# Kernel optimization log

Measured on AMD Instinct MI355X. Metric: run time of the kernel, lower is better.

## Reference

```python
import jax, jax.numpy as jnp
import numpy as np

K = 16  # top-k affinities kept per current-frame pixel (init arg k)


def setup_inputs() -> dict:
    key = jax.random.key(0)
    k1, k2 = jax.random.split(key)
    B, C, H, W = 2, 256, 64, 64
    N = H * W
    cur_prev_aff = jax.random.normal(k1, (B, N, N), dtype=jnp.float32)
    feat = jax.random.normal(k2, (B, C, H, W), dtype=jnp.float32)
    return {"cur_prev_aff": cur_prev_aff, "feat": feat}


def reference(cur_prev_aff, feat):
    # cur_prev_aff: [B, N, N] affinity from each current pixel i to each prev pixel j
    # feat:         [B, C, H, W] previous-frame features, N = H*W
    B, C, H, W = feat.shape
    N = H * W
    # top-k affinity masking per current pixel
    vals, idx = jax.lax.top_k(cur_prev_aff, K)      # [B, N, K]
    w = jax.nn.softmax(vals, axis=-1)               # normalized masked affinities (masked_cpa)
    # gather prev-frame features at top-k locations and weighted-sum
    feat_t = feat.reshape(B, C, N).transpose(0, 2, 1)        # [B, N, C]
    gathered = jax.vmap(lambda f, ix: f[ix])(feat_t, idx)    # [B, N, K, C]
    out = jnp.einsum('bnk,bnkc->bnc', w, gathered)           # [B, N, C]
    return out.transpose(0, 2, 1).reshape(B, C, H, W)
```

## Files before the change

kernel.cpp:

```cpp
#include <hip/hip_runtime.h>

#define N_PIX 4096
#define N_CH 256
#define KSEL 16

__device__ __forceinline__ unsigned f2key(float f) {
  unsigned u = __float_as_uint(f);
  return u ^ ((unsigned)((int)u >> 31) | 0x80000000u);
}
__device__ __forceinline__ float key2f(unsigned k) {
  unsigned u = (k & 0x80000000u) ? (k ^ 0x80000000u) : ~k;
  return __uint_as_float(u);
}
__device__ __forceinline__ unsigned umax2(unsigned a, unsigned b) { return a > b ? a : b; }

__global__ void transpose_feat_kernel(const float* __restrict__ feat,
                                      float* __restrict__ feat_t) {
  __shared__ float tile[32][33];
  const int b = blockIdx.z;
  const int n0 = blockIdx.x * 32;
  const int c0 = blockIdx.y * 32;
  const int tx = threadIdx.x, ty = threadIdx.y;
  const float* src = feat + (size_t)b * N_CH * N_PIX;
  float* dst = feat_t + (size_t)b * N_PIX * N_CH;
#pragma unroll
  for (int j = 0; j < 32; j += 8)
    tile[ty + j][tx] = src[(size_t)(c0 + ty + j) * N_PIX + n0 + tx];
  __syncthreads();
#pragma unroll
  for (int j = 0; j < 32; j += 8)
    dst[(size_t)(n0 + ty + j) * N_CH + c0 + tx] = tile[tx][ty + j];
}

template <bool FT>
__global__ __launch_bounds__(256, 3) void topk_wave_kernel(
    const float* __restrict__ aff, const float* __restrict__ feat,
    float* __restrict__ out) {
  __shared__ unsigned s_ck[4][64];
  __shared__ unsigned s_cj[4][64];
  __shared__ uint2 s_wj[4][KSEL];
  __shared__ float s_out[4][N_CH];

  const int tid = threadIdx.x;
  const int lane = tid & 63;
  const int w = tid >> 6;
  const int rg = blockIdx.x;
  const int b = rg >> 10;
  const int i0 = (rg & 1023) * 4;
  const int row = rg * 4 + w;
  const unsigned long long lt = (1ull << lane) - 1ull;

  const float4* arow = (const float4*)(aff + (size_t)row * N_PIX);
  unsigned key[64];
  unsigned m = 0;
#pragma unroll
  for (int q = 0; q < 16; ++q) {
    float4 v = arow[q * 64 + lane];
    unsigned k0 = f2key(v.x), k1 = f2key(v.y), k2 = f2key(v.z), k3 = f2key(v.w);
    key[4 * q + 0] = k0; key[4 * q + 1] = k1;
    key[4 * q + 2] = k2; key[4 * q + 3] = k3;
    m = umax2(m, umax2(umax2(k0, k1), umax2(k2, k3)));
  }

  unsigned p1 = 0, need1 = KSEL;
#pragma unroll
  for (int bit = 31; bit >= 0; --bit) {
    unsigned want = (p1 << 1) | 1u;
    unsigned cnt = (unsigned)__popcll(__ballot((m >> bit) == want));
    bool take = cnt >= need1;
    p1 = want - (take ? 0u : 1u);
    need1 = take ? need1 : need1 - cnt;
  }
  const unsigned T1 = p1;

  unsigned base = 0;
#pragma unroll
  for (int e = 0; e < 64; ++e) {
    bool sel = key[e] >= T1;
    unsigned long long mk = __ballot(sel);
    if (sel) {
      unsigned pos = base + (unsigned)__popcll(mk & lt);
      if (pos < 64) {
        s_ck[w][pos] = key[e];
        s_cj[w][pos] = (unsigned)((e >> 2) * 256 + lane * 4 + (e & 3));
      }
    }
    base += (unsigned)__popcll(mk);
  }

  if (__builtin_expect(base <= 64, 1)) {
    unsigned cv = 0, cj = 0xFFFFFFFFu;
    if (lane < (int)base) { cv = s_ck[w][lane]; cj = s_cj[w][lane]; }
    unsigned p2 = 0, need2 = KSEL;
#pragma unroll
    for (int bit = 31; bit >= 0; --bit) {
      unsigned want = (p2 << 1) | 1u;
      unsigned cnt = (unsigned)__popcll(__ballot((cv >> bit) == want));
      bool take = cnt >= need2;
      p2 = want - (take ? 0u : 1u);
      need2 = take ? need2 : need2 - cnt;
    }
    const unsigned T2 = p2;
    bool win = (cv > T2);
    bool eq = (cv == T2) && (lane < (int)base);
    unsigned long long eqm = __ballot(eq);
    if (need2 == (unsigned)__popcll(eqm)) {
      win = win || eq;
    } else {
      bool t = eq;
      for (unsigned q = 0; q < need2; ++q) {
        unsigned mi = t ? cj : 0xFFFFFFFFu;
#pragma unroll
        for (int off = 32; off; off >>= 1) {
          unsigned o = (unsigned)__shfl_xor((int)mi, off, 64);
          mi = o < mi ? o : mi;
        }
        if (t && cj == mi) { win = true; t = false; }
      }
    }
    unsigned long long wm = __ballot(win);
    if (win) {
      unsigned rk = (unsigned)__popcll(wm & lt);
      float ew = __expf(key2f(cv) - key2f(T2));
      s_wj[w][rk] = make_uint2(__float_as_uint(ew), cj);
    }
  } else {
    unsigned p2 = 0, need2 = KSEL;
    for (int bit = 31; bit >= 0; --bit) {
      unsigned want = (p2 << 1) | 1u;
      unsigned cnt = 0;
#pragma unroll
      for (int e = 0; e < 64; ++e)
        cnt += (unsigned)__popcll(__ballot((key[e] >> bit) == want));
      bool take = cnt >= need2;
      p2 = want - (take ? 0u : 1u);
      need2 = take ? need2 : need2 - cnt;
    }
    const unsigned T2 = p2;
    unsigned rk = 0;
#pragma unroll
    for (int e = 0; e < 64; ++e) {
      bool sel = key[e] > T2;
      unsigned long long mk = __ballot(sel);
      if (sel) {
        unsigned pos = rk + (unsigned)__popcll(mk & lt);
        float ew = __expf(key2f(key[e]) - key2f(T2));
        s_wj[w][pos] = make_uint2(__float_as_uint(ew),
                                  (unsigned)((e >> 2) * 256 + lane * 4 + (e & 3)));
      }
      rk += (unsigned)__popcll(mk);
    }
    unsigned long long done = 0ull;
    for (unsigned q = 0; q < need2; ++q) {
      unsigned mi = 0xFFFFFFFFu;
#pragma unroll
      for (int e = 0; e < 64; ++e) {
        if (key[e] == T2 && !((done >> e) & 1ull)) {
          unsigned j = (unsigned)((e >> 2) * 256 + lane * 4 + (e & 3));
          if (j < mi) mi = j;
        }
      }
      unsigned gmi = mi;
#pragma unroll
      for (int off = 32; off; off >>= 1) {
        unsigned o = (unsigned)__shfl_xor((int)gmi, off, 64);
        gmi = o < gmi ? o : gmi;
      }
      if (mi == gmi && gmi != 0xFFFFFFFFu) {
        unsigned e = ((gmi >> 8) << 2) | (gmi & 3);
        done |= (1ull << e);
        s_wj[w][rk + q] = make_uint2(__float_as_uint(1.0f), gmi);
      }
    }
  }

  float ews[KSEL];
  unsigned js[KSEL];
  float ssum = 0.f;
#pragma unroll
  for (int k = 0; k < KSEL; ++k) {
    uint2 t = s_wj[w][k];
    ews[k] = __uint_as_float(t.x);
    js[k] = t.y;
    ssum += ews[k];
  }
  const float inv = 1.0f / ssum;

  float ax = 0.f, ay = 0.f, az = 0.f, aw = 0.f;
  if (FT) {
    const float* fb = feat + (size_t)b * N_PIX * N_CH + lane * 4;
#pragma unroll
    for (int k = 0; k < KSEL; ++k) {
      const float4 f = *(const float4*)(fb + (size_t)js[k] * N_CH);
      ax += ews[k] * f.x; ay += ews[k] * f.y;
      az += ews[k] * f.z; aw += ews[k] * f.w;
    }
  } else {
    const float* fb = feat + (size_t)b * N_CH * N_PIX;
    const int c0 = lane * 4;
#pragma unroll
    for (int k = 0; k < KSEL; ++k) {
      ax += ews[k] * fb[(size_t)(c0 + 0) * N_PIX + js[k]];
      ay += ews[k] * fb[(size_t)(c0 + 1) * N_PIX + js[k]];
      az += ews[k] * fb[(size_t)(c0 + 2) * N_PIX + js[k]];
      aw += ews[k] * fb[(size_t)(c0 + 3) * N_PIX + js[k]];
    }
  }
  float4 accv;
  accv.x = ax * inv; accv.y = ay * inv; accv.z = az * inv; accv.w = aw * inv;
  *(float4*)&s_out[w][lane * 4] = accv;

  __syncthreads();

  {
    const int c = tid;
    float4 o;
    o.x = s_out[0][c]; o.y = s_out[1][c]; o.z = s_out[2][c]; o.w = s_out[3][c];
    *(float4*)(out + ((size_t)(b * N_CH + c)) * N_PIX + i0) = o;
  }
}

extern "C" void kernel_launch(void* const* d_in, const int* in_sizes, int n_in,
                              void* d_out, int out_size, void* d_ws, size_t ws_size,
                              hipStream_t stream) {
  const float* aff = (const float*)d_in[0];
  const float* feat = (const float*)d_in[1];
  float* out = (float*)d_out;
  const size_t feat_t_bytes = (size_t)2 * N_PIX * N_CH * sizeof(float);
  if (ws_size >= feat_t_bytes) {
    float* feat_t = (float*)d_ws;
    dim3 tb(32, 8, 1);
    dim3 tg(N_PIX / 32, N_CH / 32, 2);
    transpose_feat_kernel<<<tg, tb, 0, stream>>>(feat, feat_t);
    topk_wave_kernel<true><<<2048, 256, 0, stream>>>(aff, feat_t, out);
  } else {
    topk_wave_kernel<false><<<2048, 256, 0, stream>>>(aff, feat, out);
  }
}
```

Measured before the change: 49.48 us.

## Drop register-held keys, re-read affinity row in second pass for occupancy

The 64-entry per-lane key array is no longer kept in registers. The affinity row is read a second time (expected to hit cache) to collect candidates, which lets launch bounds rise to 4 blocks per CU for higher occupancy. The candidate buffer grows to 128 entries, so the fallback path runs less often. Block indices are remapped to spread rows across XCDs, and the softmax now subtracts the row max rather than the threshold. The cost is a second global read of each row and extra re-reads in the rare fallback path.

New measurement: 67.70 us. 1.37x slower.

```diff
diff --git a/kernel.cpp b/kernel.cpp
--- a/kernel.cpp
+++ b/kernel.cpp
@@ -3,6 +3,7 @@
 #define N_PIX 4096
 #define N_CH 256
 #define KSEL 16
+#define CCAP 128
 
 __device__ __forceinline__ unsigned f2key(float f) {
   unsigned u = __float_as_uint(f);
@@ -33,34 +34,38 @@
 }
 
 template <bool FT>
-__global__ __launch_bounds__(256, 3) void topk_wave_kernel(
+__global__ __launch_bounds__(256, 4) void topk_2pass_kernel(
     const float* __restrict__ aff, const float* __restrict__ feat,
     float* __restrict__ out) {
-  __shared__ unsigned s_ck[4][64];
-  __shared__ unsigned s_cj[4][64];
+  __shared__ unsigned s_ck[4][CCAP];
+  __shared__ unsigned s_cj[4][CCAP];
   __shared__ uint2 s_wj[4][KSEL];
   __shared__ float s_out[4][N_CH];
 
   const int tid = threadIdx.x;
   const int lane = tid & 63;
   const int w = tid >> 6;
-  const int rg = blockIdx.x;
+  const int bid = blockIdx.x;
+  const int rg = (bid & 7) * 256 + (bid >> 3);
   const int b = rg >> 10;
   const int i0 = (rg & 1023) * 4;
   const int row = rg * 4 + w;
   const unsigned long long lt = (1ull << lane) - 1ull;
 
   const float4* arow = (const float4*)(aff + (size_t)row * N_PIX);
-  unsigned key[64];
+
   unsigned m = 0;
 #pragma unroll
   for (int q = 0; q < 16; ++q) {
     float4 v = arow[q * 64 + lane];
-    unsigned k0 = f2key(v.x), k1 = f2key(v.y), k2 = f2key(v.z), k3 = f2key(v.w);
-    key[4 * q + 0] = k0; key[4 * q + 1] = k1;
-    key[4 * q + 2] = k2; key[4 * q + 3] = k3;
-    m = umax2(m, umax2(umax2(k0, k1), umax2(k2, k3)));
-  }
+    m = umax2(m, umax2(umax2(f2key(v.x), f2key(v.y)),
+                       umax2(f2key(v.z), f2key(v.w))));
+  }
+  unsigned km = m;
+#pragma unroll
+  for (int off = 32; off; off >>= 1)
+    km = umax2(km, (unsigned)__shfl_xor((int)km, off, 64));
+  const float vmax = key2f(km);
 
   unsigned p1 = 0, need1 = KSEL;
 #pragma unroll
@@ -73,117 +78,139 @@
   }
   const unsigned T1 = p1;
 
+  asm volatile("" ::: "memory");
+
   unsigned base = 0;
 #pragma unroll
-  for (int e = 0; e < 64; ++e) {
-    bool sel = key[e] >= T1;
-    unsigned long long mk = __ballot(sel);
-    if (sel) {
-      unsigned pos = base + (unsigned)__popcll(mk & lt);
-      if (pos < 64) {
-        s_ck[w][pos] = key[e];
-        s_cj[w][pos] = (unsigned)((e >> 2) * 256 + lane * 4 + (e & 3));
-      }
-    }
-    base += (unsigned)__popcll(mk);
-  }
-
-  if (__builtin_expect(base <= 64, 1)) {
-    unsigned cv = 0, cj = 0xFFFFFFFFu;
-    if (lane < (int)base) { cv = s_ck[w][lane]; cj = s_cj[w][lane]; }
+  for (int q = 0; q < 16; ++q) {
+    float4 v = arow[q * 64 + lane];
+    unsigned kk[4] = {f2key(v.x), f2key(v.y), f2key(v.z), f2key(v.w)};
+#pragma unroll
+    for (int c = 0; c < 4; ++c) {
+      bool sel = kk[c] >= T1;
+      unsigned long long mk = __ballot(sel);
+      if (sel) {
+        unsigned pos = base + (unsigned)__popcll(mk & lt);
+        if (pos < CCAP) {
+          s_ck[w][pos] = kk[c];
+          s_cj[w][pos] = (unsigned)(q * 256 + lane * 4 + c);
+        }
+      }
+      base += (unsigned)__popcll(mk);
+    }
+  }
+
+  if (__builtin_expect(base <= CCAP, 1)) {
+    unsigned cv0 = 0, cj0 = 0xFFFFFFFFu, cv1 = 0, cj1 = 0xFFFFFFFFu;
+    if (lane < (int)base) { cv0 = s_ck[w][lane]; cj0 = s_cj[w][lane]; }
+    if (lane + 64 < (int)base) { cv1 = s_ck[w][lane + 64]; cj1 = s_cj[w][lane + 64]; }
+
     unsigned p2 = 0, need2 = KSEL;
 #pragma unroll
     for (int bit = 31; bit >= 0; --bit) {
       unsigned want = (p2 << 1) | 1u;
-      unsigned cnt = (unsigned)__popcll(__ballot((cv >> bit) == want));
+      unsigned cnt = (unsigned)__popcll(__ballot((cv0 >> bit) == want)) +
+                     (unsigned)__popcll(__ballot((cv1 >> bit) == want));
       bool take = cnt >= need2;
       p2 = want - (take ? 0u : 1u);
       need2 = take ? need2 : need2 - cnt;
     }
     const unsigned T2 = p2;
-    bool win = (cv > T2);
-    bool eq = (cv == T2) && (lane < (int)base);
-    unsigned long long eqm = __ballot(eq);
-    if (need2 == (unsigned)__popcll(eqm)) {
-      win = win || eq;
+
+    bool win0 = cv0 > T2, win1 = cv1 > T2;
+    bool eq0 = (lane < (int)base) && (cv0 == T2);
+    bool eq1 = (lane + 64 < (int)base) && (cv1 == T2);
+    unsigned cntEq = (unsigned)__popcll(__ballot(eq0)) +
+                     (unsigned)__popcll(__ballot(eq1));
+    if (cntEq == need2) {
+      win0 = win0 || eq0;
+      win1 = win1 || eq1;
     } else {
-      bool t = eq;
+      bool t0 = eq0, t1 = eq1;
       for (unsigned q = 0; q < need2; ++q) {
-        unsigned mi = t ? cj : 0xFFFFFFFFu;
+        unsigned mi0 = t0 ? cj0 : 0xFFFFFFFFu;
+        unsigned mi1 = t1 ? cj1 : 0xFFFFFFFFu;
+        unsigned mi = mi0 < mi1 ? mi0 : mi1;
 #pragma unroll
         for (int off = 32; off; off >>= 1) {
           unsigned o = (unsigned)__shfl_xor((int)mi, off, 64);
           mi = o < mi ? o : mi;
         }
-        if (t && cj == mi) { win = true; t = false; }
-      }
-    }
-    unsigned long long wm = __ballot(win);
-    if (win) {
-      unsigned rk = (unsigned)__popcll(wm & lt);
-      float ew = __expf(key2f(cv) - key2f(T2));
-      s_wj[w][rk] = make_uint2(__float_as_uint(ew), cj);
+        if (t0 && cj0 == mi) { win0 = true; t0 = false; }
+        else if (t1 && cj1 == mi) { win1 = true; t1 = false; }
+      }
+    }
+
+    unsigned long long m0 = __ballot(win0);
+    unsigned long long m1 = __ballot(win1);
+    const unsigned n0w = (unsigned)__popcll(m0);
+    if (win0) {
+      unsigned rk = (unsigned)__popcll(m0 & lt);
+      s_wj[w][rk] = make_uint2(__float_as_uint(__expf(key2f(cv0) - vmax)), cj0);
+    }
+    if (win1) {
+      unsigned rk = n0w + (unsigned)__popcll(m1 & lt);
+      s_wj[w][rk] = make_uint2(__float_as_uint(__expf(key2f(cv1) - vmax)), cj1);
     }
   } else {
     unsigned p2 = 0, need2 = KSEL;
     for (int bit = 31; bit >= 0; --bit) {
       unsigned want = (p2 << 1) | 1u;
       unsigned cnt = 0;
-#pragma unroll
-      for (int e = 0; e < 64; ++e)
-        cnt += (unsigned)__popcll(__ballot((key[e] >> bit) == want));
+      for (int q = 0; q < 16; ++q) {
+        float4 v = arow[q * 64 + lane];
+        cnt += (unsigned)__popcll(__ballot((f2key(v.x) >> bit) == want));
+        cnt += (unsigned)__popcll(__ballot((f2key(v.y) >> bit) == want));
+        cnt += (unsigned)__popcll(__ballot((f2key(v.z) >> bit) == want));
+        cnt += (unsigned)__popcll(__ballot((f2key(v.w) >> bit) == want));
+      }
       bool take = cnt >= need2;
       p2 = want - (take ? 0u : 1u);
       need2 = take ? need2 : need2 - cnt;
     }
     const unsigned T2 = p2;
     unsigned rk = 0;
-#pragma unroll
-    for (int e = 0; e < 64; ++e) {
-      bool sel = key[e] > T2;
-      unsigned long long mk = __ballot(sel);
-      if (sel) {
-        unsigned pos = rk + (unsigned)__popcll(mk & lt);
-        float ew = __expf(key2f(key[e]) - key2f(T2));
-        s_wj[w][pos] = make_uint2(__float_as_uint(ew),
-                                  (unsigned)((e >> 2) * 256 + lane * 4 + (e & 3)));
-      }
-      rk += (unsigned)__popcll(mk);
-    }
-    unsigned long long done = 0ull;
-    for (unsigned q = 0; q < need2; ++q) {
+    for (int q = 0; q < 16; ++q) {
+      float4 v = arow[q * 64 + lane];
+      unsigned kk[4] = {f2key(v.x), f2key(v.y), f2key(v.z), f2key(v.w)};
+      for (int c = 0; c < 4; ++c) {
+        bool sel = kk[c] > T2;
+        unsigned long long mk = __ballot(sel);
+        if (sel) {
+          unsigned pos = rk + (unsigned)__popcll(mk & lt);
+          if (pos < KSEL)
+            s_wj[w][pos] = make_uint2(
+                __float_as_uint(__expf(key2f(kk[c]) - vmax)),
+                (unsigned)(q * 256 + lane * 4 + c));
+        }
+        rk += (unsigned)__popcll(mk);
+      }
+    }
+    unsigned jprev = 0xFFFFFFFFu;
+    for (unsigned t = rk; t < KSEL; ++t) {
       unsigned mi = 0xFFFFFFFFu;
-#pragma unroll
-      for (int e = 0; e < 64; ++e) {
-        if (key[e] == T2 && !((done >> e) & 1ull)) {
-          unsigned j = (unsigned)((e >> 2) * 256 + lane * 4 + (e & 3));
-          if (j < mi) mi = j;
-        }
-      }
-      unsigned gmi = mi;
+      for (int q = 0; q < 16; ++q) {
+        float4 v = arow[q * 64 + lane];
+        unsigned kk[4] = {f2key(v.x), f2key(v.y), f2key(v.z), f2key(v.w)};
+        for (int c = 0; c < 4; ++c) {
+          unsigned j = (unsigned)(q * 256 + lane * 4 + c);
+          if (kk[c] == T2 && (jprev == 0xFFFFFFFFu || j > jprev) && j < mi) mi = j;
+        }
+      }
 #pragma unroll
       for (int off = 32; off; off >>= 1) {
-        unsigned o = (unsigned)__shfl_xor((int)gmi, off, 64);
-        gmi = o < gmi ? o : gmi;
-      }
-      if (mi == gmi && gmi != 0xFFFFFFFFu) {
-        unsigned e = ((gmi >> 8) << 2) | (gmi & 3);
-        done |= (1ull << e);
-        s_wj[w][rk + q] = make_uint2(__float_as_uint(1.0f), gmi);
-      }
-    }
-  }
-
-  float ews[KSEL];
-  unsigned js[KSEL];
+        unsigned o = (unsigned)__shfl_xor((int)mi, off, 64);
+        mi = o < mi ? o : mi;
+      }
+      if (lane == 0)
+        s_wj[w][t] = make_uint2(__float_as_uint(__expf(key2f(T2) - vmax)), mi);
+      jprev = mi;
+    }
+  }
+
   float ssum = 0.f;
 #pragma unroll
-  for (int k = 0; k < KSEL; ++k) {
-    uint2 t = s_wj[w][k];
-    ews[k] = __uint_as_float(t.x);
-    js[k] = t.y;
-    ssum += ews[k];
-  }
+  for (int k = 0; k < KSEL; ++k) ssum += __uint_as_float(s_wj[w][k].x);
   const float inv = 1.0f / ssum;
 
   float ax = 0.f, ay = 0.f, az = 0.f, aw = 0.f;
@@ -191,19 +218,22 @@
     const float* fb = feat + (size_t)b * N_PIX * N_CH + lane * 4;
 #pragma unroll
     for (int k = 0; k < KSEL; ++k) {
-      const float4 f = *(const float4*)(fb + (size_t)js[k] * N_CH);
-      ax += ews[k] * f.x; ay += ews[k] * f.y;
-      az += ews[k] * f.z; aw += ews[k] * f.w;
+      uint2 t = s_wj[w][k];
+      const float ew = __uint_as_float(t.x);
+      const float4 f = *(const float4*)(fb + (size_t)t.y * N_CH);
+      ax += ew * f.x; ay += ew * f.y; az += ew * f.z; aw += ew * f.w;
     }
   } else {
     const float* fb = feat + (size_t)b * N_CH * N_PIX;
     const int c0 = lane * 4;
 #pragma unroll
     for (int k = 0; k < KSEL; ++k) {
-      ax += ews[k] * fb[(size_t)(c0 + 0) * N_PIX + js[k]];
-      ay += ews[k] * fb[(size_t)(c0 + 1) * N_PIX + js[k]];
-      az += ews[k] * fb[(size_t)(c0 + 2) * N_PIX + js[k]];
-      aw += ews[k] * fb[(size_t)(c0 + 3) * N_PIX + js[k]];
+      uint2 t = s_wj[w][k];
+      const float ew = __uint_as_float(t.x);
+      ax += ew * fb[(size_t)(c0 + 0) * N_PIX + t.y];
+      ay += ew * fb[(size_t)(c0 + 1) * N_PIX + t.y];
+      az += ew * fb[(size_t)(c0 + 2) * N_PIX + t.y];
+      aw += ew * fb[(size_t)(c0 + 3) * N_PIX + t.y];
     }
   }
   float4 accv;
@@ -232,8 +262,8 @@
     dim3 tb(32, 8, 1);
     dim3 tg(N_PIX / 32, N_CH / 32, 2);
     transpose_feat_kernel<<<tg, tb, 0, stream>>>(feat, feat_t);
-    topk_wave_kernel<true><<<2048, 256, 0, stream>>>(aff, feat_t, out);
+    topk_2pass_kernel<true><<<2048, 256, 0, stream>>>(aff, feat_t, out);
   } else {
-    topk_wave_kernel<false><<<2048, 256, 0, stream>>>(aff, feat, out);
-  }
-}
+    topk_2pass_kernel<false><<<2048, 256, 0, stream>>>(aff, feat, out);
+  }
+}
```
